# Optimization experiments

Measured on AMD Instinct MI355X. Metric: run time of the kernel, lower is better.

Reference implementation:

```python
import jax, jax.numpy as jnp
import numpy as np


def conv3d(x, w, b):
    # x: [B,C,D,H,W], w: [O,I,3,3,3], padding=1, stride=1
    y = jax.lax.conv_general_dilated(
        x, w, window_strides=(1, 1, 1), padding=[(1, 1)] * 3,
        dimension_numbers=("NCDHW", "OIDHW", "NCDHW"))
    return y + b[None, :, None, None, None]


def trilinear_sample(x, cd, ch, cw):
    # x: [B,C,D,H,W]; cd/ch/cw: [B,K,D,H,W] float sampling coords.
    # Zero padding outside the volume (invalid corners masked to 0).
    B, C, D, H, W = x.shape
    d0 = jnp.floor(cd); h0 = jnp.floor(ch); w0 = jnp.floor(cw)
    fd, fh, fw = cd - d0, ch - h0, cw - w0
    d0 = d0.astype(jnp.int32); h0 = h0.astype(jnp.int32); w0 = w0.astype(jnp.int32)
    gather = jax.vmap(lambda xb, z, y, xx: xb[:, z, y, xx])  # -> [B,C,K,D,H,W]
    out = jnp.zeros((B, C) + cd.shape[1:], x.dtype)
    for dz in (0, 1):
        wz = fd if dz else 1.0 - fd
        zi = d0 + dz
        for dy in (0, 1):
            wy = fh if dy else 1.0 - fh
            yi = h0 + dy
            for dx in (0, 1):
                wx = fw if dx else 1.0 - fw
                xi = w0 + dx
                valid = ((zi >= 0) & (zi < D) & (yi >= 0) & (yi < H)
                         & (xi >= 0) & (xi < W)).astype(x.dtype)
                v = gather(x, jnp.clip(zi, 0, D - 1), jnp.clip(yi, 0, H - 1),
                           jnp.clip(xi, 0, W - 1))
                out = out + (wz * wy * wx * valid)[:, None] * v
    return out


def deform_conv3d(x, offsets, mask, w, b):
    # Modulated deformable 3D conv (DCNv2-style), kernel 3x3x3, pad 1, stride 1.
    # offsets: [B,81,D,H,W] = 27 taps x (dd,dh,dw); mask: [B,27,D,H,W].
    B, C, D, H, W = x.shape
    K = 27
    off = offsets.reshape(B, K, 3, D, H, W)
    kd, kh, kw = jnp.meshgrid(jnp.arange(3), jnp.arange(3), jnp.arange(3), indexing="ij")
    tap_d = (kd.reshape(-1) - 1).astype(x.dtype)[None, :, None, None, None]
    tap_h = (kh.reshape(-1) - 1).astype(x.dtype)[None, :, None, None, None]
    tap_w = (kw.reshape(-1) - 1).astype(x.dtype)[None, :, None, None, None]
    gd = jnp.arange(D, dtype=x.dtype)[None, None, :, None, None]
    gh = jnp.arange(H, dtype=x.dtype)[None, None, None, :, None]
    gw = jnp.arange(W, dtype=x.dtype)[None, None, None, None, :]
    cd = gd + tap_d + off[:, :, 0]
    ch = gh + tap_h + off[:, :, 1]
    cw = gw + tap_w + off[:, :, 2]
    sampled = trilinear_sample(x, cd, ch, cw) * mask[:, None]  # [B,C,K,D,H,W]
    out = jnp.einsum("bckdhw,ock->bodhw", sampled, w.reshape(w.shape[0], C, K))
    return out + b[None, :, None, None, None]


def mdconv3d(x, ow, ob, w, b):
    # MDConv3d: internal offset/mask predictor + modulated deformable conv.
    d = conv3d(x, ow, ob)
    offsets, mask = d[:, :81], jax.nn.sigmoid(d[:, 81:])
    return deform_conv3d(x, offsets, mask, w, b)


def forward(x, ow1, ob1, w1, b1, ow2, ob2, w2, b2, ow3, ob3, w3, b3,
            defo_w, defo_b, c3d_w, c3d_b):
    h = jax.nn.relu(mdconv3d(x, ow1, ob1, w1, b1))
    h = jax.nn.relu(mdconv3d(h, ow2, ob2, w2, b2))
    h = jax.nn.relu(mdconv3d(h, ow3, ob3, w3, b3))
    d = conv3d(h, defo_w, defo_b)
    offsets, alpha = d[:, :81], jax.nn.sigmoid(d[:, 81:])
    return deform_conv3d(x, offsets, alpha, c3d_w, c3d_b)


def setup_inputs() -> dict:
    key = jax.random.key(0)
    ks = jax.random.split(key, 16)
    B, C, D, H, W = 1, 256, 8, 32, 32
    M = 256  # mdim
    OFF_SCALE = 0.02  # small init so predicted offsets stay moderate

    def p(k, shape):
        return jax.random.normal(k, shape, jnp.float32) * OFF_SCALE

    inp = {"x": jax.random.normal(ks[0], (B, C, D, H, W), jnp.float32)}
    c_ins = [C, M, M]
    for i, cin in enumerate(c_ins, 1):
        inp[f"ow{i}"] = p(ks[2 * i - 1], (108, cin, 3, 3, 3))
        inp[f"ob{i}"] = jnp.zeros((108,), jnp.float32)
        inp[f"w{i}"] = p(ks[2 * i], (M, cin, 3, 3, 3))
        inp[f"b{i}"] = jnp.zeros((M,), jnp.float32)
    inp["defo_w"] = p(ks[13], (108, M, 3, 3, 3))
    inp["defo_b"] = jnp.zeros((108,), jnp.float32)
    inp["c3d_w"] = p(ks[14], (256, C, 3, 3, 3))
    inp["c3d_b"] = jnp.zeros((256,), jnp.float32)
    return inp


def reference(x, ow1, ob1, w1, b1, ow2, ob2, w2, b2, ow3, ob3, w3, b3,
              defo_w, defo_b, c3d_w, c3d_b):
    return forward(x, ow1, ob1, w1, b1, ow2, ob2, w2, b2, ow3, ob3, w3, b3,
                   defo_w, defo_b, c3d_w, c3d_b)
```

## Files before the change

kernel.cpp:

```cpp
#include <hip/hip_runtime.h>
#include <cstdint>

#define NPOS 8192
#define KTOT 6912
#define XP_ROWS 11560
#define XP_SY 34
#define XP_SZ 1156
#define KS 4
#define KSL 1728

typedef float  facc_t __attribute__((ext_vector_type(4)));
typedef short  bf8_t  __attribute__((ext_vector_type(8)));
typedef unsigned short ub8_t __attribute__((ext_vector_type(8)));

__device__ __forceinline__ unsigned short f2bf(float f) {
    unsigned u = __float_as_uint(f);
    u = (u + 0x7FFFu + ((u >> 16) & 1u)) >> 16;
    return (unsigned short)u;
}
__device__ __forceinline__ float bf2f(unsigned short u) {
    return __uint_as_float(((unsigned)u) << 16);
}

__global__ __launch_bounds__(256) void zero_k(unsigned short* __restrict__ dst) {
    ub8_t zz = {0,0,0,0,0,0,0,0};
    *(ub8_t*)&dst[((size_t)blockIdx.x * 256 + threadIdx.x) * 8] = zz;
}

__global__ __launch_bounds__(256) void pad_x_t(const float* __restrict__ x,
                                               unsigned short* __restrict__ XpA) {
    __shared__ unsigned short T[256 * 33];
    int b = blockIdx.x;
    int z = b >> 5, y = b & 31;
    int t = threadIdx.x;
    int c8 = t >> 5, xv = t & 31;
#pragma unroll 4
    for (int i = 0; i < 32; ++i) {
        int c = i * 8 + c8;
        T[c * 33 + xv] = f2bf(x[c * NPOS + (z << 10) + (y << 5) + xv]);
    }
    __syncthreads();
    int rowb = ((z + 1) * XP_SZ + (y + 1) * XP_SY + 1) * 256;
#pragma unroll 4
    for (int j = 0; j < 32; ++j) {
        XpA[rowb + j * 256 + t] = T[t * 33 + j];
    }
}

__global__ __launch_bounds__(256) void wtrans_all(
    const float* __restrict__ o1, const float* __restrict__ o2,
    const float* __restrict__ o3, const float* __restrict__ o4,
    const float* __restrict__ m1, const float* __restrict__ m2,
    const float* __restrict__ m3, const float* __restrict__ m4,
    unsigned short* __restrict__ wtoff, unsigned short* __restrict__ wtmain) {
    __shared__ float T[6912];
    int b = blockIdx.x, t = threadIdx.x;
    const float* src; unsigned short* dst; int o, O;
    if (b < 512) {
        int L = b >> 7; o = b & 127; O = 108;
        src = (L == 0) ? o1 : (L == 1) ? o2 : (L == 2) ? o3 : o4;
        dst = wtoff + ((size_t)(L * 128 + o)) * KTOT;
    } else {
        int b2 = b - 512;
        int L = b2 >> 8; o = b2 & 255; O = 256;
        src = (L == 0) ? m1 : (L == 1) ? m2 : (L == 2) ? m3 : m4;
        dst = wtmain + ((size_t)(L * 256 + o)) * KTOT;
    }
    if (o < O) {
#pragma unroll 3
        for (int i = 0; i < 27; ++i) T[i * 256 + t] = src[(size_t)o * KTOT + i * 256 + t];
        __syncthreads();
#pragma unroll 3
        for (int i = 0; i < 27; ++i) {
            int kc = i * 256 + t;
            int c = kc & 255, k = kc >> 8;
            dst[kc] = f2bf(T[c * 27 + k]);
        }
    } else {
#pragma unroll 3
        for (int i = 0; i < 27; ++i) dst[i * 256 + t] = 0;
    }
}

template<bool DEFORM>
__global__ __launch_bounds__(256)
void fgemm(const unsigned short* __restrict__ Xp,
           const unsigned short* __restrict__ wt,
           const float* __restrict__ dbuf,
           float* __restrict__ parts) {
    constexpr int O   = DEFORM ? 256 : 128;
    constexpr int PWN = DEFORM ? 4 : 2;
    __shared__ unsigned short Bs[64 * 64] __attribute__((aligned(16)));

    const int t = threadIdx.x;
    const int wave = t >> 6, lane = t & 63;
    const int q = lane >> 4, r = lane & 15;
    const int pbase = blockIdx.x * 64;
    const int ks = blockIdx.y;
    const int kstart = ks * KSL;

    const int obw = DEFORM ? (wave * 64) : ((wave >> 1) * 64);
    const int pfb = DEFORM ? 0 : ((wave & 1) * 32);

    const int pl = t >> 2;
    const int csub = (t & 3) * 16;
    const int p = pbase + pl;
    const int z = p >> 10, y = (p >> 5) & 31, xx = p & 31;
    const int g0 = (t & 3) * 2;
    const int wr0 = pl * 64 + ((g0 ^ (pl & 7)) << 3);
    const int wr1 = pl * 64 + (((g0 + 1) ^ (pl & 7)) << 3);

    facc_t acc[4][PWN];
#pragma unroll
    for (int i = 0; i < 4; ++i)
#pragma unroll
        for (int ip = 0; ip < PWN; ++ip) acc[i][ip] = (facc_t){0.f, 0.f, 0.f, 0.f};

    float cw[8];
    int row0 = 0;
    int kprev = -1;

    for (int chunk = 0; chunk < KSL / 64; ++chunk) {
        const int kc0 = kstart + chunk * 64;
        const int k = kc0 >> 8;
        const int c0 = kc0 & 255;
        const int kd = k / 9, kh = (k / 3) % 3, kw = k % 3;

        bf8_t afr[2][4];
#pragma unroll
        for (int sl = 0; sl < 2; ++sl)
#pragma unroll
            for (int i = 0; i < 4; ++i)
                afr[sl][i] = *(const bf8_t*)&wt[(size_t)(obw + i * 16 + r) * KTOT + kc0 + sl * 32 + q * 8];

        if (DEFORM) {
            if (k != kprev) {
                kprev = k;
                float od  = dbuf[(3 * k + 0) * NPOS + p];
                float oh  = dbuf[(3 * k + 1) * NPOS + p];
                float ow_ = dbuf[(3 * k + 2) * NPOS + p];
                float m   = dbuf[(81 + k) * NPOS + p];
                float cd = (float)(z + kd - 1) + od;
                float ch = (float)(y + kh - 1) + oh;
                float cx = (float)(xx + kw - 1) + ow_;
                float fdf = floorf(cd), fhf = floorf(ch), fwf = floorf(cx);
                float fd = cd - fdf, fh = ch - fhf, fw = cx - fwf;
                float wz0 = 1.f - fd, wz1 = fd;
                float wy0 = 1.f - fh, wy1 = fh;
                float wx0 = 1.f - fw, wx1 = fw;
                int id, ih, iw;
                if (fdf < -1.f || fdf >= 8.f)  { wz0 = 0.f; wz1 = 0.f; id = 0; } else id = (int)fdf;
                if (fhf < -1.f || fhf >= 32.f) { wy0 = 0.f; wy1 = 0.f; ih = 0; } else ih = (int)fhf;
                if (fwf < -1.f || fwf >= 32.f) { wx0 = 0.f; wx1 = 0.f; iw = 0; } else iw = (int)fwf;
                wz0 *= m; wz1 *= m;
                float w00 = wz0 * wy0, w01 = wz0 * wy1, w10 = wz1 * wy0, w11 = wz1 * wy1;
                cw[0] = w00 * wx0; cw[1] = w00 * wx1;
                cw[2] = w01 * wx0; cw[3] = w01 * wx1;
                cw[4] = w10 * wx0; cw[5] = w10 * wx1;
                cw[6] = w11 * wx0; cw[7] = w11 * wx1;
                row0 = (id + 1) * XP_SZ + (ih + 1) * XP_SY + (iw + 1);
            }
            float av[16];
#pragma unroll
            for (int e = 0; e < 16; ++e) av[e] = 0.f;
            const unsigned short* cb = Xp + (size_t)row0 * 256 + c0 + csub;
#pragma unroll
            for (int j = 0; j < 8; ++j) {
                const int roff = ((j >> 2) & 1) * XP_SZ + ((j >> 1) & 1) * XP_SY + (j & 1);
                ub8_t lo = *(const ub8_t*)(cb + roff * 256);
                ub8_t hi = *(const ub8_t*)(cb + roff * 256 + 8);
#pragma unroll
                for (int e = 0; e < 8; ++e) {
                    av[e]     += cw[j] * bf2f(lo[e]);
                    av[8 + e] += cw[j] * bf2f(hi[e]);
                }
            }
            ub8_t v0, v1;
#pragma unroll
            for (int e = 0; e < 8; ++e) { v0[e] = f2bf(av[e]); v1[e] = f2bf(av[8 + e]); }
            *(ub8_t*)&Bs[wr0] = v0;
            *(ub8_t*)&Bs[wr1] = v1;
        } else {
            int row = (z + kd) * XP_SZ + (y + kh) * XP_SY + (xx + kw);
            ub8_t lo = *(const ub8_t*)&Xp[(size_t)row * 256 + c0 + csub];
            ub8_t hi = *(const ub8_t*)&Xp[(size_t)row * 256 + c0 + csub + 8];
            *(ub8_t*)&Bs[wr0] = lo;
            *(ub8_t*)&Bs[wr1] = hi;
        }
        __syncthreads();

#pragma unroll
        for (int sl = 0; sl < 2; ++sl) {
            bf8_t bfr[PWN];
#pragma unroll
            for (int ip = 0; ip < PWN; ++ip) {
                int brow = pfb + ip * 16 + r;
                bfr[ip] = *(const bf8_t*)&Bs[brow * 64 + (((sl * 4 + q) ^ (brow & 7)) << 3)];
            }
#pragma unroll
            for (int i = 0; i < 4; ++i)
#pragma unroll
                for (int ip = 0; ip < PWN; ++ip)
                    acc[i][ip] = __builtin_amdgcn_mfma_f32_16x16x32_bf16(afr[sl][i], bfr[ip], acc[i][ip], 0, 0, 0);
        }
        __syncthreads();
    }

    float* pp = parts + (size_t)ks * O * NPOS;
#pragma unroll
    for (int i = 0; i < 4; ++i)
#pragma unroll
        for (int ip = 0; ip < PWN; ++ip)
#pragma unroll
            for (int reg = 0; reg < 4; ++reg) {
                int o = obw + i * 16 + q * 4 + reg;
                int px = pbase + pfb + ip * 16 + r;
                pp[(size_t)o * NPOS + px] = acc[i][ip][reg];
            }
}

__global__ __launch_bounds__(256) void ccombine(const float* __restrict__ parts,
                                                const float* __restrict__ ob,
                                                float* __restrict__ dbuf) {
    int b = blockIdx.x;
    int o = b >> 3;
    int p4 = ((b & 7) * 256 + threadIdx.x) * 4;
    float s0 = 0, s1 = 0, s2 = 0, s3 = 0;
#pragma unroll
    for (int s = 0; s < KS; ++s) {
        const float4 v = *(const float4*)&parts[((size_t)(s * 128 + o)) * NPOS + p4];
        s0 += v.x; s1 += v.y; s2 += v.z; s3 += v.w;
    }
    float bv = ob[o];
    s0 += bv; s1 += bv; s2 += bv; s3 += bv;
    if (o >= 81) {
        s0 = 1.f / (1.f + __expf(-s0));
        s1 = 1.f / (1.f + __expf(-s1));
        s2 = 1.f / (1.f + __expf(-s2));
        s3 = 1.f / (1.f + __expf(-s3));
    }
    *(float4*)&dbuf[(size_t)o * NPOS + p4] = make_float4(s0, s1, s2, s3);
}

__global__ __launch_bounds__(256) void dcombine_h(const float* __restrict__ parts,
                                                  const float* __restrict__ bias,
                                                  unsigned short* __restrict__ XpB) {
    __shared__ unsigned short T[64 * 66];
    int p0 = blockIdx.x * 64, o0 = blockIdx.y * 64;
    int t = threadIdx.x;
    int pl = t & 63, og = t >> 6;
#pragma unroll 4
    for (int j = 0; j < 16; ++j) {
        int ol = og * 16 + j;
        float s = 0.f;
#pragma unroll
        for (int sp = 0; sp < KS; ++sp)
            s += parts[((size_t)(sp * 256 + o0 + ol)) * NPOS + p0 + pl];
        s += bias[o0 + ol];
        T[ol * 66 + pl] = f2bf(fmaxf(s, 0.f));
    }
    __syncthreads();
    int c = t & 63, pr = t >> 6;
#pragma unroll 4
    for (int j = 0; j < 16; ++j) {
        int pl2 = j * 4 + pr;
        int pg = p0 + pl2;
        int zz = pg >> 10, yy = (pg >> 5) & 31, xv = pg & 31;
        int row = (zz + 1) * XP_SZ + (yy + 1) * XP_SY + xv + 1;
        XpB[(size_t)row * 256 + o0 + c] = T[c * 66 + pl2];
    }
}

__global__ __launch_bounds__(256) void dcombine_out(const float* __restrict__ parts,
                                                    const float* __restrict__ bias,
                                                    float* __restrict__ out) {
    int b = blockIdx.x;
    int o = b >> 3;
    int p4 = ((b & 7) * 256 + threadIdx.x) * 4;
    float s0 = 0, s1 = 0, s2 = 0, s3 = 0;
#pragma unroll
    for (int s = 0; s < KS; ++s) {
        const float4 v = *(const float4*)&parts[((size_t)(s * 256 + o)) * NPOS + p4];
        s0 += v.x; s1 += v.y; s2 += v.z; s3 += v.w;
    }
    float bv = bias[o];
    *(float4*)&out[(size_t)o * NPOS + p4] = make_float4(s0 + bv, s1 + bv, s2 + bv, s3 + bv);
}

extern "C" void kernel_launch(void* const* d_in, const int* in_sizes, int n_in,
                              void* d_out, int out_size, void* d_ws, size_t ws_size,
                              hipStream_t stream) {
    const float* x      = (const float*)d_in[0];
    const float* ow1    = (const float*)d_in[1];
    const float* ob1    = (const float*)d_in[2];
    const float* w1     = (const float*)d_in[3];
    const float* b1     = (const float*)d_in[4];
    const float* ow2    = (const float*)d_in[5];
    const float* ob2    = (const float*)d_in[6];
    const float* w2     = (const float*)d_in[7];
    const float* b2     = (const float*)d_in[8];
    const float* ow3    = (const float*)d_in[9];
    const float* ob3    = (const float*)d_in[10];
    const float* w3     = (const float*)d_in[11];
    const float* b3     = (const float*)d_in[12];
    const float* defo_w = (const float*)d_in[13];
    const float* defo_b = (const float*)d_in[14];
    const float* c3d_w  = (const float*)d_in[15];
    const float* c3d_b  = (const float*)d_in[16];
    float* out = (float*)d_out;

    unsigned short* XpA    = (unsigned short*)d_ws;
    unsigned short* XpB    = XpA + (size_t)XP_ROWS * 256;
    unsigned short* wtoff  = XpB + (size_t)XP_ROWS * 256;
    unsigned short* wtmain = wtoff + (size_t)4 * 128 * KTOT;
    float* dbufp = (float*)(wtmain + (size_t)4 * 256 * KTOT);
    float* parts = dbufp + (size_t)108 * NPOS;

    const dim3 blk(256);
    const dim3 gG(128, KS);

    zero_k<<<2890, blk, 0, stream>>>(XpA);
    pad_x_t<<<256, blk, 0, stream>>>(x, XpA);
    wtrans_all<<<1536, blk, 0, stream>>>(ow1, ow2, ow3, defo_w, w1, w2, w3, c3d_w, wtoff, wtmain);

    const float* cbias[4] = {ob1, ob2, ob3, defo_b};
    const float* dbias[4] = {b1, b2, b3, c3d_b};

    for (int L = 0; L < 4; ++L) {
        const unsigned short* featConv = (L == 0) ? XpA : XpB;
        const unsigned short* featDef  = (L == 3) ? XpA : featConv;
        fgemm<false><<<gG, blk, 0, stream>>>(featConv, wtoff + (size_t)L * 128 * KTOT, nullptr, parts);
        ccombine<<<864, blk, 0, stream>>>(parts, cbias[L], dbufp);
        fgemm<true><<<gG, blk, 0, stream>>>(featDef, wtmain + (size_t)L * 256 * KTOT, dbufp, parts);
        if (L < 3) dcombine_h<<<dim3(128, 4), blk, 0, stream>>>(parts, dbias[L], XpB);
        else       dcombine_out<<<2048, blk, 0, stream>>>(parts, dbias[L], out);
    }
}
```

Before: 766.1 us.

## Double-buffer LDS staging in fgemm and raise split-K to six slices

Converts the GEMM main loop to a double-buffered software pipeline: the next chunk's weight fragments are prefetched and its B tile (including the deformable trilinear gather) is staged into the alternate LDS buffer while MFMAs run on the current one. This removes one barrier per chunk. Split-K rises from 4 to 6 to put more blocks on the GPU, and launch bounds ask for 3 blocks per CU. The column mapping of each thread's two 8-element groups changes to sub*8 and sub*8+32. The costs are more LDS and registers, and more partial sums for the combine kernel to read back.

```diff
diff --git a/kernel.cpp b/kernel.cpp
--- a/kernel.cpp
+++ b/kernel.cpp
@@ -6,8 +6,8 @@
 #define XP_ROWS 11560
 #define XP_SY 34
 #define XP_SZ 1156
-#define KS 4
-#define KSL 1728
+#define KS 6
+#define KSL 1152
 
 typedef float  facc_t __attribute__((ext_vector_type(4)));
 typedef short  bf8_t  __attribute__((ext_vector_type(8)));
@@ -83,14 +83,15 @@
 }
 
 template<bool DEFORM>
-__global__ __launch_bounds__(256)
+__global__ __launch_bounds__(256, 3)
 void fgemm(const unsigned short* __restrict__ Xp,
            const unsigned short* __restrict__ wt,
            const float* __restrict__ dbuf,
            float* __restrict__ parts) {
     constexpr int O   = DEFORM ? 256 : 128;
     constexpr int PWN = DEFORM ? 4 : 2;
-    __shared__ unsigned short Bs[64 * 64] __attribute__((aligned(16)));
+    constexpr int NCH = KSL / 64;
+    __shared__ unsigned short Bs[2][64 * 64] __attribute__((aligned(16)));
 
     const int t = threadIdx.x;
     const int wave = t >> 6, lane = t & 63;
@@ -103,39 +104,44 @@
     const int pfb = DEFORM ? 0 : ((wave & 1) * 32);
 
     const int pl = t >> 2;
-    const int csub = (t & 3) * 16;
+    const int sub = t & 3;
     const int p = pbase + pl;
     const int z = p >> 10, y = (p >> 5) & 31, xx = p & 31;
-    const int g0 = (t & 3) * 2;
-    const int wr0 = pl * 64 + ((g0 ^ (pl & 7)) << 3);
-    const int wr1 = pl * 64 + (((g0 + 1) ^ (pl & 7)) << 3);
+    const int wr_lo = pl * 64 + ((sub ^ (pl & 7)) << 3);
+    const int wr_hi = pl * 64 + (((sub + 4) ^ (pl & 7)) << 3);
+
+    const unsigned short* arow[4];
+#pragma unroll
+    for (int i = 0; i < 4; ++i)
+        arow[i] = wt + (size_t)(obw + i * 16 + r) * KTOT + q * 8;
 
     facc_t acc[4][PWN];
 #pragma unroll
     for (int i = 0; i < 4; ++i)
 #pragma unroll
-        for (int ip = 0; ip < PWN; ++ip) acc[i][ip] = (facc_t){0.f, 0.f, 0.f, 0.f};
+        for (int ip = 0; ip < PWN; ++ip) acc[ip < PWN ? i : i][ip] = (facc_t){0.f, 0.f, 0.f, 0.f};
 
     float cw[8];
     int row0 = 0;
     int kprev = -1;
 
-    for (int chunk = 0; chunk < KSL / 64; ++chunk) {
-        const int kc0 = kstart + chunk * 64;
+    auto loadA = [&](int n, bf8_t af[2][4]) {
+        const int kc0 = kstart + n * 64;
+#pragma unroll
+        for (int sl = 0; sl < 2; ++sl)
+#pragma unroll
+            for (int i = 0; i < 4; ++i)
+                af[sl][i] = *(const bf8_t*)(arow[i] + kc0 + sl * 32);
+    };
+
+    auto stage = [&](int n, int buf) {
+        const int kc0 = kstart + n * 64;
         const int k = kc0 >> 8;
         const int c0 = kc0 & 255;
-        const int kd = k / 9, kh = (k / 3) % 3, kw = k % 3;
-
-        bf8_t afr[2][4];
-#pragma unroll
-        for (int sl = 0; sl < 2; ++sl)
-#pragma unroll
-            for (int i = 0; i < 4; ++i)
-                afr[sl][i] = *(const bf8_t*)&wt[(size_t)(obw + i * 16 + r) * KTOT + kc0 + sl * 32 + q * 8];
-
         if (DEFORM) {
             if (k != kprev) {
                 kprev = k;
+                const int kd = k / 9, kh = (k / 3) % 3, kw = k % 3;
                 float od  = dbuf[(3 * k + 0) * NPOS + p];
                 float oh  = dbuf[(3 * k + 1) * NPOS + p];
                 float ow_ = dbuf[(3 * k + 2) * NPOS + p];
@@ -160,15 +166,15 @@
                 cw[6] = w11 * wx0; cw[7] = w11 * wx1;
                 row0 = (id + 1) * XP_SZ + (ih + 1) * XP_SY + (iw + 1);
             }
+            const unsigned short* cb = Xp + (size_t)row0 * 256 + c0 + sub * 8;
             float av[16];
 #pragma unroll
             for (int e = 0; e < 16; ++e) av[e] = 0.f;
-            const unsigned short* cb = Xp + (size_t)row0 * 256 + c0 + csub;
 #pragma unroll
             for (int j = 0; j < 8; ++j) {
                 const int roff = ((j >> 2) & 1) * XP_SZ + ((j >> 1) & 1) * XP_SY + (j & 1);
                 ub8_t lo = *(const ub8_t*)(cb + roff * 256);
-                ub8_t hi = *(const ub8_t*)(cb + roff * 256 + 8);
+                ub8_t hi = *(const ub8_t*)(cb + roff * 256 + 32);
 #pragma unroll
                 for (int e = 0; e < 8; ++e) {
                     av[e]     += cw[j] * bf2f(lo[e]);
@@ -178,32 +184,53 @@
             ub8_t v0, v1;
 #pragma unroll
             for (int e = 0; e < 8; ++e) { v0[e] = f2bf(av[e]); v1[e] = f2bf(av[8 + e]); }
-            *(ub8_t*)&Bs[wr0] = v0;
-            *(ub8_t*)&Bs[wr1] = v1;
+            *(ub8_t*)&Bs[buf][wr_lo] = v0;
+            *(ub8_t*)&Bs[buf][wr_hi] = v1;
         } else {
+            const int kd = k / 9, kh = (k / 3) % 3, kw = k % 3;
             int row = (z + kd) * XP_SZ + (y + kh) * XP_SY + (xx + kw);
-            ub8_t lo = *(const ub8_t*)&Xp[(size_t)row * 256 + c0 + csub];
-            ub8_t hi = *(const ub8_t*)&Xp[(size_t)row * 256 + c0 + csub + 8];
-            *(ub8_t*)&Bs[wr0] = lo;
-            *(ub8_t*)&Bs[wr1] = hi;
+            ub8_t lo = *(const ub8_t*)&Xp[(size_t)row * 256 + c0 + sub * 8];
+            ub8_t hi = *(const ub8_t*)&Xp[(size_t)row * 256 + c0 + sub * 8 + 32];
+            *(ub8_t*)&Bs[buf][wr_lo] = lo;
+            *(ub8_t*)&Bs[buf][wr_hi] = hi;
         }
-        __syncthreads();
-
+    };
+
+    auto domfma = [&](int buf, bf8_t af[2][4]) {
 #pragma unroll
         for (int sl = 0; sl < 2; ++sl) {
             bf8_t bfr[PWN];
 #pragma unroll
             for (int ip = 0; ip < PWN; ++ip) {
                 int brow = pfb + ip * 16 + r;
-                bfr[ip] = *(const bf8_t*)&Bs[brow * 64 + (((sl * 4 + q) ^ (brow & 7)) << 3)];
+                bfr[ip] = *(const bf8_t*)&Bs[buf][brow * 64 + (((sl * 4 + q) ^ (brow & 7)) << 3)];
             }
 #pragma unroll
             for (int i = 0; i < 4; ++i)
 #pragma unroll
                 for (int ip = 0; ip < PWN; ++ip)
-                    acc[i][ip] = __builtin_amdgcn_mfma_f32_16x16x32_bf16(afr[sl][i], bfr[ip], acc[i][ip], 0, 0, 0);
+                    acc[i][ip] = __builtin_amdgcn_mfma_f32_16x16x32_bf16(af[sl][i], bfr[ip], acc[i][ip], 0, 0, 0);
         }
+    };
+
+    bf8_t afr[2][4], afn[2][4];
+    loadA(0, afr);
+    stage(0, 0);
+    __syncthreads();
+
+#pragma unroll 2
+    for (int n = 0; n < NCH; ++n) {
+        const int buf = n & 1;
+        if (n + 1 < NCH) {
+            loadA(n + 1, afn);
+            stage(n + 1, buf ^ 1);
+        }
+        domfma(buf, afr);
         __syncthreads();
+#pragma unroll
+        for (int sl = 0; sl < 2; ++sl)
+#pragma unroll
+            for (int i = 0; i < 4; ++i) afr[sl][i] = afn[sl][i];
     }
 
     float* pp = parts + (size_t)ks * O * NPOS;
```

Result: slower. 1.569 ms (+104.8%).

## Double-buffer LDS staging in fused GEMM and raise split-K to six

Applied to the files above, without the earlier changes.

Turns the single LDS buffer into a ping-pong pair so the next chunk's gather or trilinear interpolation is staged while the current chunk's MFMAs run, which removes one barrier per chunk. Split-K goes from 4 to 6 slices, giving more blocks, and launch bounds request 3 blocks per CU to cap register use. The costs are more partial-sum traffic in the combine step, possible register spills under the tighter bound, and double the LDS per block.

```diff
diff --git a/kernel.cpp b/kernel.cpp
--- a/kernel.cpp
+++ b/kernel.cpp
@@ -6,8 +6,8 @@
 #define XP_ROWS 11560
 #define XP_SY 34
 #define XP_SZ 1156
-#define KS 4
-#define KSL 1728
+#define KS 6
+#define KSL 1152
 
 typedef float  facc_t __attribute__((ext_vector_type(4)));
 typedef short  bf8_t  __attribute__((ext_vector_type(8)));
@@ -83,14 +83,15 @@
 }
 
 template<bool DEFORM>
-__global__ __launch_bounds__(256)
+__global__ __launch_bounds__(256, 3)
 void fgemm(const unsigned short* __restrict__ Xp,
            const unsigned short* __restrict__ wt,
            const float* __restrict__ dbuf,
            float* __restrict__ parts) {
     constexpr int O   = DEFORM ? 256 : 128;
     constexpr int PWN = DEFORM ? 4 : 2;
-    __shared__ unsigned short Bs[64 * 64] __attribute__((aligned(16)));
+    constexpr int NCH = KSL / 64;
+    __shared__ unsigned short Bs[2][64 * 64] __attribute__((aligned(16)));
 
     const int t = threadIdx.x;
     const int wave = t >> 6, lane = t & 63;
@@ -110,6 +111,11 @@
     const int wr0 = pl * 64 + ((g0 ^ (pl & 7)) << 3);
     const int wr1 = pl * 64 + (((g0 + 1) ^ (pl & 7)) << 3);
 
+    const unsigned short* arow[4];
+#pragma unroll
+    for (int i = 0; i < 4; ++i)
+        arow[i] = wt + (size_t)(obw + i * 16 + r) * KTOT + q * 8;
+
     facc_t acc[4][PWN];
 #pragma unroll
     for (int i = 0; i < 4; ++i)
@@ -120,22 +126,14 @@
     int row0 = 0;
     int kprev = -1;
 
-    for (int chunk = 0; chunk < KSL / 64; ++chunk) {
-        const int kc0 = kstart + chunk * 64;
+    auto stage = [&](int n, int buf) {
+        const int kc0 = kstart + n * 64;
         const int k = kc0 >> 8;
         const int c0 = kc0 & 255;
-        const int kd = k / 9, kh = (k / 3) % 3, kw = k % 3;
-
-        bf8_t afr[2][4];
-#pragma unroll
-        for (int sl = 0; sl < 2; ++sl)
-#pragma unroll
-            for (int i = 0; i < 4; ++i)
-                afr[sl][i] = *(const bf8_t*)&wt[(size_t)(obw + i * 16 + r) * KTOT + kc0 + sl * 32 + q * 8];
-
         if (DEFORM) {
             if (k != kprev) {
                 kprev = k;
+                const int kd = k / 9, kh = (k / 3) % 3, kw = k % 3;
                 float od  = dbuf[(3 * k + 0) * NPOS + p];
                 float oh  = dbuf[(3 * k + 1) * NPOS + p];
                 float ow_ = dbuf[(3 * k + 2) * NPOS + p];
@@ -160,10 +158,10 @@
                 cw[6] = w11 * wx0; cw[7] = w11 * wx1;
                 row0 = (id + 1) * XP_SZ + (ih + 1) * XP_SY + (iw + 1);
             }
+            const unsigned short* cb = Xp + (size_t)row0 * 256 + c0 + csub;
             float av[16];
 #pragma unroll
             for (int e = 0; e < 16; ++e) av[e] = 0.f;
-            const unsigned short* cb = Xp + (size_t)row0 * 256 + c0 + csub;
 #pragma unroll
             for (int j = 0; j < 8; ++j) {
                 const int roff = ((j >> 2) & 1) * XP_SZ + ((j >> 1) & 1) * XP_SY + (j & 1);
@@ -178,32 +176,49 @@
             ub8_t v0, v1;
 #pragma unroll
             for (int e = 0; e < 8; ++e) { v0[e] = f2bf(av[e]); v1[e] = f2bf(av[8 + e]); }
-            *(ub8_t*)&Bs[wr0] = v0;
-            *(ub8_t*)&Bs[wr1] = v1;
+            *(ub8_t*)&Bs[buf][wr0] = v0;
+            *(ub8_t*)&Bs[buf][wr1] = v1;
         } else {
+            const int kd = k / 9, kh = (k / 3) % 3, kw = k % 3;
             int row = (z + kd) * XP_SZ + (y + kh) * XP_SY + (xx + kw);
             ub8_t lo = *(const ub8_t*)&Xp[(size_t)row * 256 + c0 + csub];
             ub8_t hi = *(const ub8_t*)&Xp[(size_t)row * 256 + c0 + csub + 8];
-            *(ub8_t*)&Bs[wr0] = lo;
-            *(ub8_t*)&Bs[wr1] = hi;
+            *(ub8_t*)&Bs[buf][wr0] = lo;
+            *(ub8_t*)&Bs[buf][wr1] = hi;
+        }
+    };
+
+    auto chunkstep = [&](int n, int buf, bool doStageNext) {
+        const int kc0 = kstart + n * 64;
+        bf8_t af[2][4];
+#pragma unroll
+        for (int sl = 0; sl < 2; ++sl)
+#pragma unroll
+            for (int i = 0; i < 4; ++i)
+                af[sl][i] = *(const bf8_t*)(arow[i] + kc0 + sl * 32);
+        if (doStageNext) stage(n + 1, buf ^ 1);
+#pragma unroll
+        for (int sl = 0; sl < 2; ++sl) {
+            bf8_t bfr[PWN];
+#pragma unroll
+            for (int ip = 0; ip < PWN; ++ip) {
+                int brow = pfb + ip * 16 + r;
+                bfr[ip] = *(const bf8_t*)&Bs[buf][brow * 64 + (((sl * 4 + q) ^ (brow & 7)) << 3)];
+            }
+#pragma unroll
+            for (int i = 0; i < 4; ++i)
+#pragma unroll
+                for (int ip = 0; ip < PWN; ++ip)
+                    acc[i][ip] = __builtin_amdgcn_mfma_f32_16x16x32_bf16(af[sl][i], bfr[ip], acc[i][ip], 0, 0, 0);
         }
         __syncthreads();
-
-#pragma unroll
-        for (int sl = 0; sl < 2; ++sl) {
-            bf8_t bfr[PWN];
-#pragma unroll
-            for (int ip = 0; ip < PWN; ++ip) {
-                int brow = pfb + ip * 16 + r;
-                bfr[ip] = *(const bf8_t*)&Bs[brow * 64 + (((sl * 4 + q) ^ (brow & 7)) << 3)];
-            }
-#pragma unroll
-            for (int i = 0; i < 4; ++i)
-#pragma unroll
-                for (int ip = 0; ip < PWN; ++ip)
-                    acc[i][ip] = __builtin_amdgcn_mfma_f32_16x16x32_bf16(afr[sl][i], bfr[ip], acc[i][ip], 0, 0, 0);
-        }
-        __syncthreads();
+    };
+
+    stage(0, 0);
+    __syncthreads();
+    for (int n = 0; n < NCH; n += 2) {
+        chunkstep(n, 0, true);
+        chunkstep(n + 1, 1, n + 2 < NCH);
     }
 
     float* pp = parts + (size_t)ks * O * NPOS;
```

Result: slower. 1.711 ms (+123.3%).
